# Kernel optimization log

Measured on AMD Instinct MI355X. Metric: run time of the kernel, lower is better.

The kernel has to match this reference:

```python
import jax, jax.numpy as jnp
import numpy as np

B, L, D = 2, 1024, 512          # batch, seq_len, d_model
H, DK, DV, P = 8, 64, 64, 4     # heads, d_k, d_v, num masks
TEMP = DK ** 0.5
EPS = 1e-6


def setup_inputs() -> dict:
    key = jax.random.key(0)
    ks = jax.random.split(key, 11)
    s = 0.04  # ~xavier scale for these fan sizes
    q = jax.random.normal(ks[0], (B, L, D), jnp.float32)
    k = jax.random.normal(ks[1], (B, L, D), jnp.float32)
    v = jax.random.normal(ks[2], (B, L, D), jnp.float32)
    mask = (jax.random.uniform(ks[3], (P, 1, 1, L, L)) > 0.2).astype(jnp.float32)
    w_q = jax.random.normal(ks[4], (H * DK, D), jnp.float32) * s
    w_k = jax.random.normal(ks[5], (H * DK, D), jnp.float32) * s
    w_v = jax.random.normal(ks[6], (H * DV, D), jnp.float32) * s
    fc_w = jax.random.normal(ks[7], (D, H * DV), jnp.float32) * s
    fc_b = jnp.zeros((D,), jnp.float32)
    ln_g = jnp.ones((D,), jnp.float32)
    ln_b = jnp.zeros((D,), jnp.float32)
    return {"q": q, "k": k, "v": v, "mask": mask, "w_q": w_q, "w_k": w_k,
            "w_v": w_v, "fc_w": fc_w, "fc_b": fc_b, "ln_g": ln_g, "ln_b": ln_b}


def reference(q, k, v, mask, w_q, w_k, w_v, fc_w, fc_b, ln_g, ln_b):
    b, lq = q.shape[0], q.shape[1]
    lk = k.shape[1]
    residual = q
    # pre-LayerNorm on q (normalize_before=True)
    mu = jnp.mean(q, axis=-1, keepdims=True)
    var = jnp.mean(jnp.square(q - mu), axis=-1, keepdims=True)
    qn = (q - mu) * jax.lax.rsqrt(var + EPS) * ln_g + ln_b
    # projections -> [B,H,L,dk/dv]
    qh = jnp.einsum('bld,ed->ble', qn, w_q).reshape(b, lq, H, DK).transpose(0, 2, 1, 3)
    kh = jnp.einsum('bld,ed->ble', k, w_k).reshape(b, lk, H, DK).transpose(0, 2, 1, 3)
    vh = jnp.einsum('bld,ed->ble', v, w_v).reshape(b, lk, H, DV).transpose(0, 2, 1, 3)
    # shared scores, computed once: [B,H,Lq,Lk]
    attn = jnp.einsum('bhqd,bhkd->bhqk', qh / TEMP, kh)
    # per-mask additive bias, vectorized over P (dropout is identity in eval)
    ext = (1.0 - mask) * -10000.0                      # [P,1,1,Lq,Lk]
    probs = jax.nn.softmax(attn[None] + ext, axis=-1)  # [P,B,H,Lq,Lk]
    out = jnp.einsum('pbhqk,bhkd->pbhqd', probs, vh)   # [P,B,H,Lq,DV]
    out = out.transpose(0, 1, 3, 2, 4).reshape(P, b, lq, H * DV)
    out = jnp.einsum('pble,de->pbld', out, fc_w) + fc_b
    out = out + residual[None]
    return (out, attn)
```

## Files before the change

kernel.cpp:

```cpp
#include <hip/hip_runtime.h>
#include <math.h>

namespace {

constexpr int B = 2, L = 1024, D = 512, H = 8, DK = 64, DV = 64, P = 4;
constexpr float EPS = 1e-6f;
constexpr float ESHIFT = 16.0f;

typedef float f32x4 __attribute__((ext_vector_type(4)));
typedef short s16x8 __attribute__((ext_vector_type(8)));

__device__ inline unsigned short f2bf(float x) {
  union { float f; unsigned u; } v; v.f = x;
  unsigned r = v.u + 0x7fffu + ((v.u >> 16) & 1u);
  return (unsigned short)(r >> 16);
}

__global__ __launch_bounds__(256) void ln_kernel(
    const float* __restrict__ x, const float* __restrict__ g,
    const float* __restrict__ bta, unsigned short* __restrict__ y) {
  int row = blockIdx.x;
  const float* xr = x + (size_t)row * D;
  unsigned short* yr = y + (size_t)row * D;
  int t = threadIdx.x;
  float v0 = xr[t], v1 = xr[t + 256];
  float s = v0 + v1;
#pragma unroll
  for (int off = 32; off; off >>= 1) s += __shfl_down(s, off, 64);
  __shared__ float red[4];
  if ((t & 63) == 0) red[t >> 6] = s;
  __syncthreads();
  float mu = (red[0] + red[1] + red[2] + red[3]) * (1.0f / D);
  float d0 = v0 - mu, d1 = v1 - mu;
  float vs = d0 * d0 + d1 * d1;
#pragma unroll
  for (int off = 32; off; off >>= 1) vs += __shfl_down(vs, off, 64);
  __syncthreads();
  if ((t & 63) == 0) red[t >> 6] = vs;
  __syncthreads();
  float var = (red[0] + red[1] + red[2] + red[3]) * (1.0f / D);
  float rstd = rsqrtf(var + EPS);
  yr[t] = f2bf(d0 * rstd * g[t] + bta[t]);
  yr[t + 256] = f2bf(d1 * rstd * g[t + 256] + bta[t + 256]);
}

struct Cvt7 {
  const float* s[7];
  unsigned short* d[7];
  int cum[8];
};
__global__ __launch_bounds__(256) void cvt7_kernel(Cvt7 a) {
  int e4 = (blockIdx.x * 256 + threadIdx.x) * 4;
  int t = 0;
  while (e4 >= a.cum[t + 1]) ++t;
  int off = e4 - a.cum[t];
  float4 v = *(const float4*)(a.s[t] + off);
  ushort4 o;
  if (t == 6) {
    o.x = v.x != 0.0f ? 0xFFFFu : 0u;
    o.y = v.y != 0.0f ? 0xFFFFu : 0u;
    o.z = v.z != 0.0f ? 0xFFFFu : 0u;
    o.w = v.w != 0.0f ? 0xFFFFu : 0u;
  } else {
    o.x = f2bf(v.x); o.y = f2bf(v.y); o.z = f2bf(v.z); o.w = f2bf(v.w);
  }
  *(ushort4*)(a.d[t] + off) = o;
}

template <bool BF16OUT, bool EXPOUT>
__global__ __launch_bounds__(256) void bgemm_nt(
    const unsigned short* __restrict__ A, int lda, long sA0, long sA1,
    const unsigned short* __restrict__ Bm, int ldb, long sB0, long sB1,
    void* __restrict__ Cv, int ldc, long sC0, long sC1,
    int Z0, int K, float alpha,
    const float* __restrict__ bias, const float* __restrict__ resid, int rm,
    unsigned short* __restrict__ Eout) {
  int z = blockIdx.z;
  int z0 = z % Z0, z1 = z / Z0;
  A += (size_t)z0 * sA0 + (size_t)z1 * sA1;
  Bm += (size_t)z0 * sB0 + (size_t)z1 * sB1;
  size_t cOff = (size_t)z0 * sC0 + (size_t)z1 * sC1;
  int m0 = blockIdx.y * 128, n0 = blockIdx.x * 128;
  int t = threadIdx.x;
  int w = t >> 6, lane = t & 63, q4 = lane >> 4, ln16 = lane & 15;
  int wm = (w >> 1) * 64, wn = (w & 1) * 64;
  __shared__ __align__(16) unsigned short As[2][128][40];
  __shared__ __align__(16) unsigned short Bs[2][128][40];
  f32x4 acc[4][4];
#pragma unroll
  for (int i = 0; i < 4; ++i)
#pragma unroll
    for (int j = 0; j < 4; ++j)
#pragma unroll
      for (int r = 0; r < 4; ++r) acc[i][j][r] = 0.0f;
  int c0 = t, c1 = t + 256;
  const unsigned short* Ar0 = A + (size_t)(m0 + (c0 >> 2)) * lda + (c0 & 3) * 8;
  const unsigned short* Ar1 = A + (size_t)(m0 + (c1 >> 2)) * lda + (c1 & 3) * 8;
  const unsigned short* Br0 = Bm + (size_t)(n0 + (c0 >> 2)) * ldb + (c0 & 3) * 8;
  const unsigned short* Br1 = Bm + (size_t)(n0 + (c1 >> 2)) * ldb + (c1 & 3) * 8;
  {
    float4 a0 = *(const float4*)Ar0;
    float4 a1 = *(const float4*)Ar1;
    float4 b0 = *(const float4*)Br0;
    float4 b1 = *(const float4*)Br1;
    *(float4*)&As[0][c0 >> 2][(c0 & 3) * 8] = a0;
    *(float4*)&As[0][c1 >> 2][(c1 & 3) * 8] = a1;
    *(float4*)&Bs[0][c0 >> 2][(c0 & 3) * 8] = b0;
    *(float4*)&Bs[0][c1 >> 2][(c1 & 3) * 8] = b1;
  }
  int nIt = K >> 5;
  for (int it = 0; it < nIt; ++it) {
    int cur = it & 1;
    float4 na0, na1, nb0, nb1;
    if (it + 1 < nIt) {
      int kt = (it + 1) * 32;
      na0 = *(const float4*)(Ar0 + kt);
      na1 = *(const float4*)(Ar1 + kt);
      nb0 = *(const float4*)(Br0 + kt);
      nb1 = *(const float4*)(Br1 + kt);
    }
    __syncthreads();
    s16x8 af[4], bf[4];
#pragma unroll
    for (int mi = 0; mi < 4; ++mi)
      af[mi] = *(const s16x8*)&As[cur][wm + mi * 16 + ln16][q4 * 8];
#pragma unroll
    for (int ni = 0; ni < 4; ++ni)
      bf[ni] = *(const s16x8*)&Bs[cur][wn + ni * 16 + ln16][q4 * 8];
#pragma unroll
    for (int mi = 0; mi < 4; ++mi)
#pragma unroll
      for (int ni = 0; ni < 4; ++ni)
        acc[mi][ni] = __builtin_amdgcn_mfma_f32_16x16x32_bf16(
            af[mi], bf[ni], acc[mi][ni], 0, 0, 0);
    if (it + 1 < nIt) {
      int nb = 1 - cur;
      *(float4*)&As[nb][c0 >> 2][(c0 & 3) * 8] = na0;
      *(float4*)&As[nb][c1 >> 2][(c1 & 3) * 8] = na1;
      *(float4*)&Bs[nb][c0 >> 2][(c0 & 3) * 8] = nb0;
      *(float4*)&Bs[nb][c1 >> 2][(c1 & 3) * 8] = nb1;
    }
  }
#pragma unroll
  for (int mi = 0; mi < 4; ++mi)
#pragma unroll
    for (int r = 0; r < 4; ++r) {
      int row = m0 + wm + mi * 16 + q4 * 4 + r;
#pragma unroll
      for (int ni = 0; ni < 4; ++ni) {
        int col = n0 + wn + ni * 16 + ln16;
        float v = acc[mi][ni][r] * alpha;
        if (bias) v += bias[col];
        if (resid) v += resid[(size_t)(row & rm) * ldc + col];
        if (BF16OUT)
          ((unsigned short*)Cv)[cOff + (size_t)row * ldc + col] = f2bf(v);
        else
          ((float*)Cv)[cOff + (size_t)row * ldc + col] = v;
        if (EXPOUT)
          Eout[cOff + (size_t)row * ldc + col] = f2bf(__expf(v - ESHIFT));
      }
    }
}

__global__ __launch_bounds__(256) void vtrans(
    const unsigned short* __restrict__ vh, unsigned short* __restrict__ vt) {
  int bh = blockIdx.y, l0 = blockIdx.x * 64;
  int b = bh >> 3, h = bh & 7;
  __shared__ __align__(16) unsigned short T[64][72];
  int t = threadIdx.x;
  int lr = t >> 2, k16 = (t & 3) * 16;
  const unsigned short* src =
      vh + (size_t)(b * L + l0 + lr) * 512 + h * 64 + k16;
  float4 x0 = *(const float4*)src;
  float4 x1 = *(const float4*)(src + 8);
  *(float4*)&T[lr][k16] = x0;
  *(float4*)&T[lr][k16 + 8] = x1;
  __syncthreads();
  int dv = t >> 2, l16 = (t & 3) * 16;
  union { unsigned short u[16]; float4 f[2]; } o;
#pragma unroll
  for (int j = 0; j < 16; ++j) o.u[j] = T[l16 + j][dv];
  unsigned short* dst = vt + (size_t)(bh * 64 + dv) * 1024 + l0 + l16;
  *(float4*)dst = o.f[0];
  *(float4*)(dst + 8) = o.f[1];
}

__global__ __launch_bounds__(512) void pmv_kernel(
    const unsigned short* __restrict__ E, const unsigned short* __restrict__ mb,
    const unsigned short* __restrict__ vt, unsigned short* __restrict__ outh) {
  int q0 = blockIdx.x * 64, bh = blockIdx.y;
  int b = bh >> 3, h = bh & 7;
  __shared__ __align__(16) unsigned short EMs[2][4][64][72];
  __shared__ __align__(16) unsigned short Vs[2][64][72];
  int t = threadIdx.x;
  int w = t >> 6, lane = t & 63, q4 = lane >> 4, ln16 = lane & 15;
  int p = w & 3, kh = (w >> 2) * 32;
  int er = t >> 3, ek = (t & 7) * 8;
  const unsigned short* erow = E + ((size_t)bh * L + q0 + er) * L + ek;
  const unsigned short* mrow = mb + (size_t)(q0 + er) * L + ek;
  const unsigned short* vsrc = vt + ((size_t)bh * 64 + er) * L + ek;
  s16x8 ones;
#pragma unroll
  for (int j = 0; j < 8; ++j) ones[j] = (short)0x3F80;
  f32x4 acc[4][4], accs[4];
#pragma unroll
  for (int i = 0; i < 4; ++i) {
#pragma unroll
    for (int r = 0; r < 4; ++r) accs[i][r] = 0.0f;
#pragma unroll
    for (int j = 0; j < 4; ++j)
#pragma unroll
      for (int r = 0; r < 4; ++r) acc[i][j][r] = 0.0f;
  }
  {
    int4 e4 = *(const int4*)erow;
    int4 vv = *(const int4*)vsrc;
#pragma unroll
    for (int pp = 0; pp < 4; ++pp) {
      int4 m4 = *(const int4*)(mrow + (size_t)pp * L * L);
      int4 em;
      em.x = e4.x & m4.x; em.y = e4.y & m4.y;
      em.z = e4.z & m4.z; em.w = e4.w & m4.w;
      *(int4*)&EMs[0][pp][er][ek] = em;
    }
    *(int4*)&Vs[0][er][ek] = vv;
  }
  for (int it = 0; it < 16; ++it) {
    int cur = it & 1;
    int4 ne, nm[4], nv;
    if (it < 15) {
      int kc = (it + 1) * 64;
      ne = *(const int4*)(erow + kc);
#pragma unroll
      for (int pp = 0; pp < 4; ++pp)
        nm[pp] = *(const int4*)(mrow + (size_t)pp * L * L + kc);
      nv = *(const int4*)(vsrc + kc);
    }
    __syncthreads();
    s16x8 af[4], bf[4];
#pragma unroll
    for (int mi = 0; mi < 4; ++mi)
      af[mi] = *(const s16x8*)&EMs[cur][p][mi * 16 + ln16][kh + q4 * 8];
#pragma unroll
    for (int ni = 0; ni < 4; ++ni)
      bf[ni] = *(const s16x8*)&Vs[cur][ni * 16 + ln16][kh + q4 * 8];
#pragma unroll
    for (int mi = 0; mi < 4; ++mi) {
#pragma unroll
      for (int ni = 0; ni < 4; ++ni)
        acc[mi][ni] = __builtin_amdgcn_mfma_f32_16x16x32_bf16(
            af[mi], bf[ni], acc[mi][ni], 0, 0, 0);
      accs[mi] = __builtin_amdgcn_mfma_f32_16x16x32_bf16(af[mi], ones,
                                                         accs[mi], 0, 0, 0);
    }
    if (it < 15) {
      int nb = cur ^ 1;
#pragma unroll
      for (int pp = 0; pp < 4; ++pp) {
        int4 em;
        em.x = ne.x & nm[pp].x; em.y = ne.y & nm[pp].y;
        em.z = ne.z & nm[pp].z; em.w = ne.w & nm[pp].w;
        *(int4*)&EMs[nb][pp][er][ek] = em;
      }
      *(int4*)&Vs[nb][er][ek] = nv;
    }
  }
  __syncthreads();
  float* sc1 = (float*)&EMs[0][0][0][0];
  float* sc2 = (float*)&Vs[0][0][0];
  int wl = (w & 3) * 64 + lane;
  if (w >= 4) {
#pragma unroll
    for (int mi = 0; mi < 4; ++mi) {
#pragma unroll
      for (int ni = 0; ni < 4; ++ni)
#pragma unroll
        for (int r = 0; r < 4; ++r)
          sc1[((mi * 4 + ni) * 4 + r) * 257 + wl] = acc[mi][ni][r];
#pragma unroll
      for (int r = 0; r < 4; ++r)
        sc2[(mi * 4 + r) * 257 + wl] = accs[mi][r];
    }
  }
  __syncthreads();
  if (w < 4) {
#pragma unroll
    for (int mi = 0; mi < 4; ++mi) {
#pragma unroll
      for (int ni = 0; ni < 4; ++ni)
#pragma unroll
        for (int r = 0; r < 4; ++r)
          acc[mi][ni][r] += sc1[((mi * 4 + ni) * 4 + r) * 257 + wl];
#pragma unroll
      for (int r = 0; r < 4; ++r)
        accs[mi][r] += sc2[(mi * 4 + r) * 257 + wl];
    }
#pragma unroll
    for (int mi = 0; mi < 4; ++mi)
#pragma unroll
      for (int r = 0; r < 4; ++r) {
        int row = mi * 16 + q4 * 4 + r;
        float inv = 1.0f / accs[mi][r];
        size_t o = ((size_t)(p * B + b) * L + q0 + row) * 512 + h * 64 + ln16;
#pragma unroll
        for (int ni = 0; ni < 4; ++ni)
          outh[o + ni * 16] = f2bf(acc[mi][ni][r] * inv);
      }
  }
}

}

extern "C" void kernel_launch(void* const* d_in, const int* in_sizes, int n_in,
                              void* d_out, int out_size, void* d_ws,
                              size_t ws_size, hipStream_t stream) {
  const float* q = (const float*)d_in[0];
  const float* k = (const float*)d_in[1];
  const float* v = (const float*)d_in[2];
  const float* mask = (const float*)d_in[3];
  const float* w_q = (const float*)d_in[4];
  const float* w_k = (const float*)d_in[5];
  const float* w_v = (const float*)d_in[6];
  const float* fc_w = (const float*)d_in[7];
  const float* fc_b = (const float*)d_in[8];
  const float* ln_g = (const float*)d_in[9];
  const float* ln_b = (const float*)d_in[10];

  float* out = (float*)d_out;
  float* attn = out + (size_t)P * B * L * D;

  unsigned short* wsu = (unsigned short*)d_ws;
  const size_t T1 = (size_t)B * L * D;
  const size_t TW = (size_t)D * D;
  unsigned short* qkv_bf = wsu;
  unsigned short* w_bf = qkv_bf + 3 * T1;
  unsigned short* fcw_bf = w_bf + 3 * TW;
  unsigned short* qh_bf = fcw_bf + TW;
  unsigned short* vt = qh_bf + 3 * T1;
  unsigned short* outh = vt + T1;
  unsigned short* mask_us = outh + 4 * T1;
  unsigned short* Ebuf = mask_us + 4 * T1;

  ln_kernel<<<B * L, 256, 0, stream>>>(q, ln_g, ln_b, qkv_bf);

  Cvt7 ca;
  ca.s[0] = k; ca.s[1] = v; ca.s[2] = w_q; ca.s[3] = w_k; ca.s[4] = w_v;
  ca.s[5] = fc_w; ca.s[6] = mask;
  ca.d[0] = qkv_bf + T1; ca.d[1] = qkv_bf + 2 * T1;
  ca.d[2] = w_bf; ca.d[3] = w_bf + TW; ca.d[4] = w_bf + 2 * TW;
  ca.d[5] = fcw_bf; ca.d[6] = mask_us;
  ca.cum[0] = 0;
  int sizes[7] = {(int)T1, (int)T1, (int)TW, (int)TW, (int)TW, (int)TW,
                  P * L * L};
  for (int i = 0; i < 7; ++i) ca.cum[i + 1] = ca.cum[i] + sizes[i];
  cvt7_kernel<<<ca.cum[7] / 1024, 256, 0, stream>>>(ca);

  bgemm_nt<true, false><<<dim3(D / 128, (B * L) / 128, 3), 256, 0, stream>>>(
      qkv_bf, D, (long)T1, 0, w_bf, D, (long)TW, 0, qh_bf, D, (long)T1, 0,
      3, D, 1.0f, nullptr, nullptr, 0, nullptr);

  vtrans<<<dim3(L / 64, B * H), 256, 0, stream>>>(qh_bf + 2 * T1, vt);

  bgemm_nt<false, true><<<dim3(L / 128, L / 128, B * H), 256, 0, stream>>>(
      qh_bf, D, 64, (long)L * D, qh_bf + T1, D, 64, (long)L * D,
      attn, L, (long)L * L, (long)H * L * L, H, DK, 0.125f, nullptr, nullptr,
      0, Ebuf);

  pmv_kernel<<<dim3(L / 64, B * H), 512, 0, stream>>>(Ebuf, mask_us, vt, outh);

  bgemm_nt<false, false><<<dim3(D / 128, (P * B * L) / 128, 1), 256, 0, stream>>>(
      outh, D, 0, 0, fcw_bf, D, 0, 0, out, D, 0, 0, 1, D, 1.0f, fc_b, q,
      B * L - 1, nullptr);
}
```

Baseline: 207.6 us.

## Fuse QK score computation into masked PV kernel and merge prep kernels

The separate QK^T GEMM that wrote fp32 scores plus a bf16 exp buffer is removed. Its work moves into the attention kernel: warps compute 64-key score chunks two iterations ahead, write fp32 attn to global and exp values into a double-buffered shared tile, and the masked PV MFMA loop reads from that tile. This avoids writing and re-reading the full exp buffer from global memory. LayerNorm and the conversion kernel are also merged into one launch. In exchange the attention kernel carries extra shared memory and registers and an uneven per-warp QK schedule, which could lower occupancy.

```diff
diff --git a/kernel.cpp b/kernel.cpp
--- a/kernel.cpp
+++ b/kernel.cpp
@@ -14,34 +14,6 @@
   union { float f; unsigned u; } v; v.f = x;
   unsigned r = v.u + 0x7fffu + ((v.u >> 16) & 1u);
   return (unsigned short)(r >> 16);
-}
-
-__global__ __launch_bounds__(256) void ln_kernel(
-    const float* __restrict__ x, const float* __restrict__ g,
-    const float* __restrict__ bta, unsigned short* __restrict__ y) {
-  int row = blockIdx.x;
-  const float* xr = x + (size_t)row * D;
-  unsigned short* yr = y + (size_t)row * D;
-  int t = threadIdx.x;
-  float v0 = xr[t], v1 = xr[t + 256];
-  float s = v0 + v1;
-#pragma unroll
-  for (int off = 32; off; off >>= 1) s += __shfl_down(s, off, 64);
-  __shared__ float red[4];
-  if ((t & 63) == 0) red[t >> 6] = s;
-  __syncthreads();
-  float mu = (red[0] + red[1] + red[2] + red[3]) * (1.0f / D);
-  float d0 = v0 - mu, d1 = v1 - mu;
-  float vs = d0 * d0 + d1 * d1;
-#pragma unroll
-  for (int off = 32; off; off >>= 1) vs += __shfl_down(vs, off, 64);
-  __syncthreads();
-  if ((t & 63) == 0) red[t >> 6] = vs;
-  __syncthreads();
-  float var = (red[0] + red[1] + red[2] + red[3]) * (1.0f / D);
-  float rstd = rsqrtf(var + EPS);
-  yr[t] = f2bf(d0 * rstd * g[t] + bta[t]);
-  yr[t + 256] = f2bf(d1 * rstd * g[t + 256] + bta[t + 256]);
 }
 
 struct Cvt7 {
@@ -49,32 +21,59 @@
   unsigned short* d[7];
   int cum[8];
 };
-__global__ __launch_bounds__(256) void cvt7_kernel(Cvt7 a) {
-  int e4 = (blockIdx.x * 256 + threadIdx.x) * 4;
-  int t = 0;
-  while (e4 >= a.cum[t + 1]) ++t;
-  int off = e4 - a.cum[t];
-  float4 v = *(const float4*)(a.s[t] + off);
-  ushort4 o;
-  if (t == 6) {
-    o.x = v.x != 0.0f ? 0xFFFFu : 0u;
-    o.y = v.y != 0.0f ? 0xFFFFu : 0u;
-    o.z = v.z != 0.0f ? 0xFFFFu : 0u;
-    o.w = v.w != 0.0f ? 0xFFFFu : 0u;
+
+__global__ __launch_bounds__(256) void prep_kernel(
+    const float* __restrict__ x, const float* __restrict__ g,
+    const float* __restrict__ bta, unsigned short* __restrict__ y, Cvt7 a) {
+  int bid = blockIdx.x, t = threadIdx.x;
+  if (bid < B * L) {
+    const float* xr = x + (size_t)bid * D;
+    unsigned short* yr = y + (size_t)bid * D;
+    float v0 = xr[t], v1 = xr[t + 256];
+    float s = v0 + v1;
+#pragma unroll
+    for (int off = 32; off; off >>= 1) s += __shfl_down(s, off, 64);
+    __shared__ float red[4];
+    if ((t & 63) == 0) red[t >> 6] = s;
+    __syncthreads();
+    float mu = (red[0] + red[1] + red[2] + red[3]) * (1.0f / D);
+    float d0 = v0 - mu, d1 = v1 - mu;
+    float vs = d0 * d0 + d1 * d1;
+#pragma unroll
+    for (int off = 32; off; off >>= 1) vs += __shfl_down(vs, off, 64);
+    __syncthreads();
+    if ((t & 63) == 0) red[t >> 6] = vs;
+    __syncthreads();
+    float var = (red[0] + red[1] + red[2] + red[3]) * (1.0f / D);
+    float rstd = rsqrtf(var + EPS);
+    yr[t] = f2bf(d0 * rstd * g[t] + bta[t]);
+    yr[t + 256] = f2bf(d1 * rstd * g[t + 256] + bta[t + 256]);
   } else {
-    o.x = f2bf(v.x); o.y = f2bf(v.y); o.z = f2bf(v.z); o.w = f2bf(v.w);
-  }
-  *(ushort4*)(a.d[t] + off) = o;
-}
-
-template <bool BF16OUT, bool EXPOUT>
+    int e4 = ((bid - B * L) * 256 + t) * 4;
+    int ti = 0;
+    while (e4 >= a.cum[ti + 1]) ++ti;
+    int off = e4 - a.cum[ti];
+    float4 v = *(const float4*)(a.s[ti] + off);
+    ushort4 o;
+    if (ti == 6) {
+      o.x = v.x != 0.0f ? 0xFFFFu : 0u;
+      o.y = v.y != 0.0f ? 0xFFFFu : 0u;
+      o.z = v.z != 0.0f ? 0xFFFFu : 0u;
+      o.w = v.w != 0.0f ? 0xFFFFu : 0u;
+    } else {
+      o.x = f2bf(v.x); o.y = f2bf(v.y); o.z = f2bf(v.z); o.w = f2bf(v.w);
+    }
+    *(ushort4*)(a.d[ti] + off) = o;
+  }
+}
+
+template <bool BF16OUT>
 __global__ __launch_bounds__(256) void bgemm_nt(
     const unsigned short* __restrict__ A, int lda, long sA0, long sA1,
     const unsigned short* __restrict__ Bm, int ldb, long sB0, long sB1,
     void* __restrict__ Cv, int ldc, long sC0, long sC1,
     int Z0, int K, float alpha,
-    const float* __restrict__ bias, const float* __restrict__ resid, int rm,
-    unsigned short* __restrict__ Eout) {
+    const float* __restrict__ bias, const float* __restrict__ resid, int rm) {
   int z = blockIdx.z;
   int z0 = z % Z0, z1 = z / Z0;
   A += (size_t)z0 * sA0 + (size_t)z1 * sA1;
@@ -156,8 +155,6 @@
           ((unsigned short*)Cv)[cOff + (size_t)row * ldc + col] = f2bf(v);
         else
           ((float*)Cv)[cOff + (size_t)row * ldc + col] = v;
-        if (EXPOUT)
-          Eout[cOff + (size_t)row * ldc + col] = f2bf(__expf(v - ESHIFT));
       }
     }
 }
@@ -185,20 +182,26 @@
   *(float4*)(dst + 8) = o.f[1];
 }
 
-__global__ __launch_bounds__(512) void pmv_kernel(
-    const unsigned short* __restrict__ E, const unsigned short* __restrict__ mb,
-    const unsigned short* __restrict__ vt, unsigned short* __restrict__ outh) {
+__global__ __launch_bounds__(512) void fattn_kernel(
+    const unsigned short* __restrict__ qh, const unsigned short* __restrict__ khm,
+    const unsigned short* __restrict__ mb, const unsigned short* __restrict__ vt,
+    float* __restrict__ attn, unsigned short* __restrict__ outh) {
   int q0 = blockIdx.x * 64, bh = blockIdx.y;
   int b = bh >> 3, h = bh & 7;
   __shared__ __align__(16) unsigned short EMs[2][4][64][72];
   __shared__ __align__(16) unsigned short Vs[2][64][72];
+  __shared__ __align__(16) unsigned short Es[2][64][72];
+  __shared__ __align__(16) unsigned short Qs[64][72];
   int t = threadIdx.x;
   int w = t >> 6, lane = t & 63, q4 = lane >> 4, ln16 = lane & 15;
-  int p = w & 3, kh = (w >> 2) * 32;
+  int p = w & 3, kh32 = (w >> 2) * 32;
+  int qw = w & 3, nlo = (w >> 2) * 2;
   int er = t >> 3, ek = (t & 7) * 8;
-  const unsigned short* erow = E + ((size_t)bh * L + q0 + er) * L + ek;
   const unsigned short* mrow = mb + (size_t)(q0 + er) * L + ek;
   const unsigned short* vsrc = vt + ((size_t)bh * 64 + er) * L + ek;
+  const unsigned short* kbase = khm + (size_t)(b * L) * 512 + h * 64;
+  float* arow = attn + (size_t)bh * L * L + (size_t)q0 * L;
+
   s16x8 ones;
 #pragma unroll
   for (int j = 0; j < 8; ++j) ones[j] = (short)0x3F80;
@@ -212,60 +215,118 @@
 #pragma unroll
       for (int r = 0; r < 4; ++r) acc[i][j][r] = 0.0f;
   }
+  s16x8 kreg[2][2];
+  int4 m4[4], v4;
+
+#define KLOAD(dd)                                                              \
+  do {                                                                         \
+    int kc_ = (dd) * 64;                                                       \
+    const unsigned short* kb_ =                                                \
+        kbase + (size_t)(kc_ + nlo * 16 + ln16) * 512 + q4 * 8;                \
+    kreg[0][0] = *(const s16x8*)kb_;                                           \
+    kreg[0][1] = *(const s16x8*)(kb_ + 32);                                    \
+    kreg[1][0] = *(const s16x8*)(kb_ + 16 * 512);                              \
+    kreg[1][1] = *(const s16x8*)(kb_ + 16 * 512 + 32);                         \
+  } while (0)
+
+#define QKCHUNK(dd)                                                            \
+  do {                                                                         \
+    f32x4 a2[4][2];                                                            \
+    _Pragma("unroll") for (int mi = 0; mi < 4; ++mi)                           \
+        _Pragma("unroll") for (int j = 0; j < 2; ++j)                          \
+            _Pragma("unroll") for (int r = 0; r < 4; ++r) a2[mi][j][r] = 0.0f; \
+    _Pragma("unroll") for (int kk = 0; kk < 2; ++kk)                           \
+        _Pragma("unroll") for (int mi = 0; mi < 4; ++mi) {                     \
+      s16x8 qf = *(const s16x8*)&Qs[mi * 16 + ln16][kk * 32 + q4 * 8];         \
+      a2[mi][0] = __builtin_amdgcn_mfma_f32_16x16x32_bf16(qf, kreg[0][kk],     \
+                                                          a2[mi][0], 0, 0, 0); \
+      a2[mi][1] = __builtin_amdgcn_mfma_f32_16x16x32_bf16(qf, kreg[1][kk],     \
+                                                          a2[mi][1], 0, 0, 0); \
+    }                                                                          \
+    int kc_ = (dd) * 64, eb_ = (dd) & 1;                                       \
+    _Pragma("unroll") for (int mi = 0; mi < 4; ++mi)                           \
+        _Pragma("unroll") for (int r = 0; r < 4; ++r) {                        \
+      int row_ = mi * 16 + q4 * 4 + r;                                         \
+      _Pragma("unroll") for (int j = 0; j < 2; ++j) {                          \
+        int col_ = (nlo + j) * 16 + ln16;                                      \
+        float v_ = a2[mi][j][r] * 0.125f;                                      \
+        arow[(size_t)row_ * L + kc_ + col_] = v_;                              \
+        Es[eb_][row_][col_] = f2bf(__expf(v_ - ESHIFT));                       \
+      }                                                                        \
+    }                                                                          \
+  } while (0)
+
   {
-    int4 e4 = *(const int4*)erow;
-    int4 vv = *(const int4*)vsrc;
+    const unsigned short* qrow =
+        qh + (size_t)(b * L + q0 + er) * 512 + h * 64 + ek;
+    *(int4*)&Qs[er][ek] = *(const int4*)qrow;
+  }
+#pragma unroll
+  for (int pp = 0; pp < 4; ++pp)
+    m4[pp] = *(const int4*)(mrow + (size_t)pp * L * L);
+  v4 = *(const int4*)vsrc;
+  KLOAD(qw);
+  __syncthreads();
+  if (qw == 0) QKCHUNK(0);
+  else if (qw == 1) QKCHUNK(1);
+  __syncthreads();
+  {
+    int4 e4 = *(const int4*)&Es[0][er][ek];
 #pragma unroll
     for (int pp = 0; pp < 4; ++pp) {
-      int4 m4 = *(const int4*)(mrow + (size_t)pp * L * L);
       int4 em;
-      em.x = e4.x & m4.x; em.y = e4.y & m4.y;
-      em.z = e4.z & m4.z; em.w = e4.w & m4.w;
+      em.x = e4.x & m4[pp].x; em.y = e4.y & m4[pp].y;
+      em.z = e4.z & m4[pp].z; em.w = e4.w & m4[pp].w;
       *(int4*)&EMs[0][pp][er][ek] = em;
     }
-    *(int4*)&Vs[0][er][ek] = vv;
-  }
-  for (int it = 0; it < 16; ++it) {
-    int cur = it & 1;
-    int4 ne, nm[4], nv;
-    if (it < 15) {
-      int kc = (it + 1) * 64;
-      ne = *(const int4*)(erow + kc);
+    *(int4*)&Vs[0][er][ek] = v4;
+  }
+  __syncthreads();
+
+  for (int c = 0; c < 16; ++c) {
+    int buf = c & 1;
+    if (c < 15) {
+      int kc = (c + 1) * 64;
 #pragma unroll
       for (int pp = 0; pp < 4; ++pp)
-        nm[pp] = *(const int4*)(mrow + (size_t)pp * L * L + kc);
-      nv = *(const int4*)(vsrc + kc);
-    }
-    __syncthreads();
-    s16x8 af[4], bf[4];
+        m4[pp] = *(const int4*)(mrow + (size_t)pp * L * L + kc);
+      v4 = *(const int4*)(vsrc + kc);
+    }
+    if (c + 4 <= 15 && ((c + 4) & 3) == qw) KLOAD(c + 4);
+    s16x8 af[4], bfv[4];
 #pragma unroll
     for (int mi = 0; mi < 4; ++mi)
-      af[mi] = *(const s16x8*)&EMs[cur][p][mi * 16 + ln16][kh + q4 * 8];
+      af[mi] = *(const s16x8*)&EMs[buf][p][mi * 16 + ln16][kh32 + q4 * 8];
 #pragma unroll
     for (int ni = 0; ni < 4; ++ni)
-      bf[ni] = *(const s16x8*)&Vs[cur][ni * 16 + ln16][kh + q4 * 8];
+      bfv[ni] = *(const s16x8*)&Vs[buf][ni * 16 + ln16][kh32 + q4 * 8];
 #pragma unroll
     for (int mi = 0; mi < 4; ++mi) {
 #pragma unroll
       for (int ni = 0; ni < 4; ++ni)
         acc[mi][ni] = __builtin_amdgcn_mfma_f32_16x16x32_bf16(
-            af[mi], bf[ni], acc[mi][ni], 0, 0, 0);
+            af[mi], bfv[ni], acc[mi][ni], 0, 0, 0);
       accs[mi] = __builtin_amdgcn_mfma_f32_16x16x32_bf16(af[mi], ones,
                                                          accs[mi], 0, 0, 0);
     }
-    if (it < 15) {
-      int nb = cur ^ 1;
+    if (c + 2 <= 15 && ((c + 2) & 3) == qw) QKCHUNK(c + 2);
+    if (c < 15) {
+      int nb = buf ^ 1;
+      int4 e4 = *(const int4*)&Es[nb][er][ek];
 #pragma unroll
       for (int pp = 0; pp < 4; ++pp) {
         int4 em;
-        em.x = ne.x & nm[pp].x; em.y = ne.y & nm[pp].y;
-        em.z = ne.z & nm[pp].z; em.w = ne.w & nm[pp].w;
+        em.x = e4.x & m4[pp].x; em.y = e4.y & m4[pp].y;
+        em.z = e4.z & m4[pp].z; em.w = e4.w & m4[pp].w;
         *(int4*)&EMs[nb][pp][er][ek] = em;
       }
-      *(int4*)&Vs[nb][er][ek] = nv;
-    }
-  }
-  __syncthreads();
+      *(int4*)&Vs[nb][er][ek] = v4;
+    }
+    __syncthreads();
+  }
+#undef KLOAD
+#undef QKCHUNK
+
   float* sc1 = (float*)&EMs[0][0][0][0];
   float* sc2 = (float*)&Vs[0][0][0];
   int wl = (w & 3) * 64 + lane;
@@ -339,9 +400,6 @@
   unsigned short* vt = qh_bf + 3 * T1;
   unsigned short* outh = vt + T1;
   unsigned short* mask_us = outh + 4 * T1;
-  unsigned short* Ebuf = mask_us + 4 * T1;
-
-  ln_kernel<<<B * L, 256, 0, stream>>>(q, ln_g, ln_b, qkv_bf);
 
   Cvt7 ca;
   ca.s[0] = k; ca.s[1] = v; ca.s[2] = w_q; ca.s[3] = w_k; ca.s[4] = w_v;
@@ -353,22 +411,19 @@
   int sizes[7] = {(int)T1, (int)T1, (int)TW, (int)TW, (int)TW, (int)TW,
                   P * L * L};
   for (int i = 0; i < 7; ++i) ca.cum[i + 1] = ca.cum[i] + sizes[i];
-  cvt7_kernel<<<ca.cum[7] / 1024, 256, 0, stream>>>(ca);
-
-  bgemm_nt<true, false><<<dim3(D / 128, (B * L) / 128, 3), 256, 0, stream>>>(
+  prep_kernel<<<B * L + ca.cum[7] / 1024, 256, 0, stream>>>(q, ln_g, ln_b,
+                                                            qkv_bf, ca);
+
+  bgemm_nt<true><<<dim3(D / 128, (B * L) / 128, 3), 256, 0, stream>>>(
       qkv_bf, D, (long)T1, 0, w_bf, D, (long)TW, 0, qh_bf, D, (long)T1, 0,
-      3, D, 1.0f, nullptr, nullptr, 0, nullptr);
+      3, D, 1.0f, nullptr, nullptr, 0);
 
   vtrans<<<dim3(L / 64, B * H), 256, 0, stream>>>(qh_bf + 2 * T1, vt);
 
-  bgemm_nt<false, true><<<dim3(L / 128, L / 128, B * H), 256, 0, stream>>>(
-      qh_bf, D, 64, (long)L * D, qh_bf + T1, D, 64, (long)L * D,
-      attn, L, (long)L * L, (long)H * L * L, H, DK, 0.125f, nullptr, nullptr,
-      0, Ebuf);
-
-  pmv_kernel<<<dim3(L / 64, B * H), 512, 0, stream>>>(Ebuf, mask_us, vt, outh);
-
-  bgemm_nt<false, false><<<dim3(D / 128, (P * B * L) / 128, 1), 256, 0, stream>>>(
+  fattn_kernel<<<dim3(L / 64, B * H), 512, 0, stream>>>(
+      qh_bf, qh_bf + T1, mask_us, vt, attn, outh);
+
+  bgemm_nt<false><<<dim3(D / 128, (P * B * L) / 128, 1), 256, 0, stream>>>(
       outh, D, 0, 0, fcw_bf, D, 0, 0, out, D, 0, 0, 1, D, 1.0f, fc_b, q,
-      B * L - 1, nullptr);
-}
+      B * L - 1);
+}
```

Result: no change. 205.6 us (-1.0%).
